# Performance work log

Hardware: AMD Instinct MI355X
Metric: run time of the kernel (lower is better)

The kernel has to match this reference:

```python
import jax, jax.numpy as jnp
import numpy as np


def setup_inputs() -> dict:
    key = jax.random.key(0)
    k1, k2 = jax.random.split(key)
    B, C_in, H, Wd = 8, 64, 64, 64
    C_a = 32
    x = jax.random.normal(k1, (B, C_in, H, Wd), dtype=jnp.float32)
    # 1x1 conv == per-pixel linear map: weight [C_a, C_in], bias [C_a]
    W = jax.random.normal(k2, (C_a, C_in), dtype=jnp.float32) * (1.0 / np.sqrt(C_in))
    b = jnp.zeros((C_a,), dtype=jnp.float32)
    return {"x": x, "W": W, "b": b}


def reference(x, W, b):
    B, C, H, Wd = x.shape
    N = H * Wd
    # g = 1x1 conv: [B, C_a, H, W] -> flatten spatial -> [B, C_a, N]
    g = jnp.einsum('oc,bchw->bohw', W, x) + b[None, :, None, None]
    g = g.reshape(B, -1, N)
    # alpha[b, n, m] = softmax_m( sum_c g[b,c,n] * g[b,c,m] )  (unscaled)
    scores = jnp.einsum('bcn,bcm->bnm', g, g)
    alpha = jax.nn.softmax(scores, axis=2)
    # r[b, c, n] = sum_m alpha[b,n,m] * x[b,c,m]
    xf = x.reshape(B, C, N)
    r = jnp.einsum('bnm,bcm->bcn', alpha, xf)
    # residual (intended semantics of is_residual=True) + ReLU epilogue
    r = r + xf
    out = jax.nn.relu(r).reshape(B, C, H, Wd)
    return (out, alpha)
```

## Files before the change

### kernel.cpp

```cpp
#include <hip/hip_runtime.h>
#include <math.h>

#define BB 8
#define CC 64
#define NA 4096
#define KA 32
#define LOG2E 1.4426950408889634f

typedef short bfrag __attribute__((ext_vector_type(8)));
typedef int   i4    __attribute__((ext_vector_type(4)));
typedef float f4    __attribute__((ext_vector_type(4)));
typedef float f16v  __attribute__((ext_vector_type(16)));

__device__ __forceinline__ f16v mf(bfrag a, bfrag b, f16v c) {
    return __builtin_amdgcn_mfma_f32_32x32x16_bf16(a, b, c, 0, 0, 0);
}

__device__ __forceinline__ unsigned short bfrne(float f) {
    unsigned u = __builtin_bit_cast(unsigned, f);
    return (unsigned short)((u + 0x7FFFu + ((u >> 16) & 1u)) >> 16);
}
__device__ __forceinline__ unsigned pk2(float a, float b) {
    return (unsigned)bfrne(a) | ((unsigned)bfrne(b) << 16);
}
__device__ __forceinline__ float bf2f(unsigned short h) {
    unsigned u = ((unsigned)h) << 16;
    return __builtin_bit_cast(float, u);
}

__global__ __launch_bounds__(256) void k_g(const float* __restrict__ x,
                                           const float* __restrict__ W,
                                           const float* __restrict__ bias,
                                           short* __restrict__ ghi,
                                           short* __restrict__ glo,
                                           float* __restrict__ norms) {
    __shared__ float Wl[KA * CC];
    __shared__ float bl[KA];
    int tid = threadIdx.x;
    for (int i = tid; i < KA * CC; i += 256) Wl[i] = W[i];
    if (tid < KA) bl[tid] = bias[tid];
    __syncthreads();

    int b = blockIdx.y;
    int n = blockIdx.x * 256 + tid;

    float acc[KA];
#pragma unroll
    for (int k = 0; k < KA; k++) acc[k] = 0.f;

    const float* xp = x + (size_t)b * CC * NA + n;
#pragma unroll 4
    for (int c = 0; c < CC; c++) {
        float xv = xp[(size_t)c * NA];
#pragma unroll
        for (int k = 0; k < KA; k++) acc[k] = fmaf(Wl[k * CC + c], xv, acc[k]);
    }

    float ss = 0.f;
    unsigned ph[KA / 2], pl[KA / 2];
#pragma unroll
    for (int k = 0; k < KA; k += 2) {
        float v0 = acc[k] + bl[k];
        float v1 = acc[k + 1] + bl[k + 1];
        ss = fmaf(v0, v0, fmaf(v1, v1, ss));
        unsigned short h0 = bfrne(v0), h1 = bfrne(v1);
        float l0 = v0 - bf2f(h0), l1 = v1 - bf2f(h1);
        ph[k / 2] = (unsigned)h0 | ((unsigned)h1 << 16);
        pl[k / 2] = (unsigned)bfrne(l0) | ((unsigned)bfrne(l1) << 16);
    }
    norms[b * NA + n] = sqrtf(ss);

    size_t row = ((size_t)b * NA + n) * KA;
#pragma unroll
    for (int q = 0; q < 4; q++) {
        i4 vh = { (int)ph[4 * q], (int)ph[4 * q + 1], (int)ph[4 * q + 2], (int)ph[4 * q + 3] };
        i4 vl = { (int)pl[4 * q], (int)pl[4 * q + 1], (int)pl[4 * q + 2], (int)pl[4 * q + 3] };
        *(i4*)(ghi + row + q * 8) = vh;
        *(i4*)(glo + row + q * 8) = vl;
    }
}

__global__ __launch_bounds__(256) void k_gmax(const float* __restrict__ norms,
                                              float* __restrict__ gmaxp) {
    int b = blockIdx.x, tid = threadIdx.x;
    float m = 0.f;
    for (int i = tid; i < NA; i += 256) m = fmaxf(m, norms[b * NA + i]);
#pragma unroll
    for (int off = 1; off < 64; off <<= 1) m = fmaxf(m, __shfl_xor(m, off));
    __shared__ float red[4];
    if ((tid & 63) == 0) red[tid >> 6] = m;
    __syncthreads();
    if (tid == 0) gmaxp[b] = fmaxf(fmaxf(red[0], red[1]), fmaxf(red[2], red[3]));
}

__global__ __launch_bounds__(256) void k_xb(const float* __restrict__ x,
                                            short* __restrict__ xb) {
    size_t idx = ((size_t)blockIdx.x * 256 + threadIdx.x) * 4;
    f4 v = *(const f4*)(x + idx);
    int2 p;
    p.x = (int)pk2(v[0], v[1]);
    p.y = (int)pk2(v[2], v[3]);
    *(int2*)(xb + idx) = p;
}

__global__ __launch_bounds__(256, 4) void k_den(const short* __restrict__ ghi,
                                                const short* __restrict__ glo,
                                                const float* __restrict__ norms,
                                                const float* __restrict__ gmaxp,
                                                float* __restrict__ partial) {
    __shared__ float rowsum[4][32];
    const int tid = threadIdx.x;
    const int w = tid >> 6;
    const int l31 = tid & 31;
    const int hi = (tid >> 5) & 1;
    const int id = blockIdx.x;
    const int b = id & 7;
    const int rr = id >> 3;
    const int nb = rr & 127;
    const int mc = rr >> 7;
    const int n0 = nb * 32;

    const float C2 = -norms[b * NA + n0 + l31] * gmaxp[b] * LOG2E;
    const short* gh = ghi + (size_t)b * NA * KA;
    const short* gl = glo + (size_t)b * NA * KA;

    bfrag Bh[2], Bl[2];
#pragma unroll
    for (int kt = 0; kt < 2; kt++) {
        size_t o = (size_t)(n0 + l31) * KA + kt * 16 + hi * 8;
        Bh[kt] = *(const bfrag*)(gh + o);
        Bl[kt] = *(const bfrag*)(gl + o);
    }

    float ls = 0.f;
#pragma unroll 2
    for (int i = 0; i < 8; i++) {
        const int m0 = (mc * 8 + i) * 128 + w * 32;
        bfrag Ah[2], Al[2];
#pragma unroll
        for (int kt = 0; kt < 2; kt++) {
            size_t o = (size_t)(m0 + l31) * KA + kt * 16 + hi * 8;
            Ah[kt] = *(const bfrag*)(gh + o);
            Al[kt] = *(const bfrag*)(gl + o);
        }
        f16v sA = {}, sB = {};
        sA = mf(Ah[0], Bh[0], sA); sA = mf(Ah[1], Bh[1], sA);
        sB = mf(Ah[0], Bl[0], sB); sB = mf(Ah[1], Bl[1], sB);
        sB = mf(Al[0], Bh[0], sB); sB = mf(Al[1], Bh[1], sB);
#pragma unroll
        for (int r = 0; r < 16; r++) ls += exp2f(fmaf(sA[r] + sB[r], LOG2E, C2));
    }
    ls += __shfl_xor(ls, 32);
    if (hi == 0) rowsum[w][l31] = ls;
    __syncthreads();
    if (tid < 32)
        partial[((size_t)mc * BB + b) * NA + n0 + tid] =
            rowsum[0][tid] + rowsum[1][tid] + rowsum[2][tid] + rowsum[3][tid];
}

__global__ __launch_bounds__(256) void k_red(const float* __restrict__ partial,
                                             float* __restrict__ linv) {
    int i = blockIdx.x * 256 + threadIdx.x;
    const size_t S = (size_t)BB * NA;
    linv[i] = 1.f / (partial[i] + partial[S + i] + partial[2 * S + i] + partial[3 * S + i]);
}

__global__ __launch_bounds__(256, 2) void k_attn2(const float* __restrict__ x,
                                                  const short* __restrict__ ghi,
                                                  const short* __restrict__ glo,
                                                  const short* __restrict__ xb,
                                                  const float* __restrict__ norms,
                                                  const float* __restrict__ gmaxp,
                                                  const float* __restrict__ linv,
                                                  float* __restrict__ out,
                                                  float* __restrict__ alpha) {
    __shared__ __align__(16) char smem[2 * 32 * 256 * 4];
    float* ast = (float*)smem;

    const int tid = threadIdx.x;
    const int w = tid >> 6;
    const int l31 = tid & 31;
    const int hi = (tid >> 5) & 1;
    const int id = blockIdx.x;
    const int b = id & 7;
    const int n0 = (id >> 3) * 32;

    const float M = norms[b * NA + n0 + l31] * gmaxp[b];
    const float C2 = -M * LOG2E;
    const float L = linv[b * NA + n0 + l31];

    const short* gh = ghi + (size_t)b * NA * KA;
    const short* gl = glo + (size_t)b * NA * KA;
    const short* xp = xb + (size_t)b * CC * NA;
    float* ap = alpha + (size_t)b * NA * NA;

    bfrag Bh[2], Bl[2];
#pragma unroll
    for (int kt = 0; kt < 2; kt++) {
        size_t o = (size_t)(n0 + l31) * KA + kt * 16 + hi * 8;
        Bh[kt] = *(const bfrag*)(gh + o);
        Bl[kt] = *(const bfrag*)(gl + o);
    }

    f16v pv0 = {}, pv1 = {};

    for (int it = 0; it < 16; ++it) {
        float* astb = ast + (it & 1) * 8192;

#pragma unroll
        for (int sub = 0; sub < 2; ++sub) {
            const int m0 = it * 256 + sub * 128 + w * 32;
            bfrag Ah[2], Al[2];
#pragma unroll
            for (int kt = 0; kt < 2; kt++) {
                size_t o = (size_t)(m0 + l31) * KA + kt * 16 + hi * 8;
                Ah[kt] = *(const bfrag*)(gh + o);
                Al[kt] = *(const bfrag*)(gl + o);
            }
            f16v sA = {}, sB = {};
            sA = mf(Ah[0], Bh[0], sA); sA = mf(Ah[1], Bh[1], sA);
            sB = mf(Ah[0], Bl[0], sB); sB = mf(Ah[1], Bl[1], sB);
            sB = mf(Al[0], Bh[0], sB); sB = mf(Al[1], Bh[1], sB);

            float a[16];
#pragma unroll
            for (int r = 0; r < 16; r++) a[r] = exp2f(fmaf(sA[r] + sB[r], LOG2E, C2)) * L;

#pragma unroll
            for (int q = 0; q < 4; q++) {
                f4 v = { a[4 * q], a[4 * q + 1], a[4 * q + 2], a[4 * q + 3] };
                int phys = (w * 8 + 2 * q + hi) ^ (l31 & 7);
                *(f4*)&astb[l31 * 256 + sub * 128 + phys * 4] = v;
            }

            unsigned p0 = pk2(a[0], a[1]),   p1 = pk2(a[2], a[3]);
            unsigned p2 = pk2(a[4], a[5]),   p3 = pk2(a[6], a[7]);
            unsigned p4 = pk2(a[8], a[9]),   p5 = pk2(a[10], a[11]);
            unsigned p6 = pk2(a[12], a[13]), p7 = pk2(a[14], a[15]);
            asm("v_permlane32_swap_b32 %0, %1" : "+v"(p0), "+v"(p2));
            asm("v_permlane32_swap_b32 %0, %1" : "+v"(p1), "+v"(p3));
            asm("v_permlane32_swap_b32 %0, %1" : "+v"(p4), "+v"(p6));
            asm("v_permlane32_swap_b32 %0, %1" : "+v"(p5), "+v"(p7));
            i4 f0 = { (int)p0, (int)p1, (int)p2, (int)p3 };
            i4 f1 = { (int)p4, (int)p5, (int)p6, (int)p7 };
            bfrag pa0 = __builtin_bit_cast(bfrag, f0);
            bfrag pa1 = __builtin_bit_cast(bfrag, f1);

            size_t ox0 = (size_t)l31 * NA + m0 + hi * 8;
            size_t ox1 = (size_t)(32 + l31) * NA + m0 + hi * 8;
            bfrag X00 = *(const bfrag*)(xp + ox0);
            bfrag X01 = *(const bfrag*)(xp + ox0 + 16);
            bfrag X10 = *(const bfrag*)(xp + ox1);
            bfrag X11 = *(const bfrag*)(xp + ox1 + 16);

            pv0 = mf(pa0, X00, pv0); pv0 = mf(pa1, X01, pv0);
            pv1 = mf(pa0, X10, pv1); pv1 = mf(pa1, X11, pv1);
        }

        __syncthreads();

#pragma unroll
        for (int e = 0; e < 8; e++) {
            int flat = e * 256 + tid;
            int row = flat >> 6;
            int c4 = flat & 63;
            int grp = c4 >> 5, c32 = c4 & 31;
            int phys = c32 ^ (row & 7);
            f4 v = *(const f4*)&astb[row * 256 + grp * 128 + phys * 4];
            __builtin_nontemporal_store(v, (f4*)(ap + (size_t)(n0 + row) * NA + it * 256 + c4 * 4));
        }
    }
    __syncthreads();

    float (*pvr0)[CC + 1] = (float(*)[CC + 1])smem;
    float (*pvr1)[CC + 1] = (float(*)[CC + 1])(smem + 32 * (CC + 1) * 4);
    if (w >= 2) {
        float (*buf)[CC + 1] = (w == 2) ? pvr0 : pvr1;
#pragma unroll
        for (int r = 0; r < 16; r++) {
            int nl = (r & 3) + 8 * (r >> 2) + 4 * hi;
            buf[nl][l31]      = pv0[r];
            buf[nl][32 + l31] = pv1[r];
        }
    }
    __syncthreads();
    if (w < 2) {
        float (*buf)[CC + 1] = (w == 0) ? pvr0 : pvr1;
#pragma unroll
        for (int r = 0; r < 16; r++) {
            int nl = (r & 3) + 8 * (r >> 2) + 4 * hi;
            buf[nl][l31]      += pv0[r];
            buf[nl][32 + l31] += pv1[r];
        }
    }
    __syncthreads();

    const float* xr = x + (size_t)b * CC * NA + n0;
    float* op = out + (size_t)b * CC * NA + n0;
#pragma unroll
    for (int e = 0; e < 8; e++) {
        int idx = e * 256 + tid;
        int c = idx >> 5, n = idx & 31;
        float v = pvr0[n][c] + pvr1[n][c] + xr[(size_t)c * NA + n];
        op[(size_t)c * NA + n] = fmaxf(v, 0.f);
    }
}

extern "C" void kernel_launch(void* const* d_in, const int* in_sizes, int n_in,
                              void* d_out, int out_size, void* d_ws, size_t ws_size,
                              hipStream_t stream) {
    const float* x = (const float*)d_in[0];
    const float* W = (const float*)d_in[1];
    const float* bias = (const float*)d_in[2];

    float* out = (float*)d_out;
    float* alpha = out + (size_t)BB * CC * NA;

    short* ghi = (short*)d_ws;
    short* glo = ghi + (size_t)BB * NA * KA;
    short* xb  = glo + (size_t)BB * NA * KA;
    float* norms = (float*)(xb + (size_t)BB * CC * NA);
    float* gmaxp = norms + (size_t)BB * NA;
    float* partial = gmaxp + BB;
    float* linv = partial + (size_t)4 * BB * NA;

    k_g<<<dim3(NA / 256, BB), 256, 0, stream>>>(x, W, bias, ghi, glo, norms);
    k_gmax<<<BB, 256, 0, stream>>>(norms, gmaxp);
    k_xb<<<(BB * CC * NA) / (256 * 4), 256, 0, stream>>>(x, xb);
    k_den<<<4096, 256, 0, stream>>>(ghi, glo, norms, gmaxp, partial);
    k_red<<<BB * NA / 256, 256, 0, stream>>>(partial, linv);
    k_attn2<<<1024, 256, 0, stream>>>(x, ghi, glo, xb, norms, gmaxp, linv, out, alpha);
}
```

Baseline: 201.4 us.

## Store alpha directly from registers, drop LDS staging, prefetch fragments, fold scale into exponent

The attention kernel no longer stages alpha tiles through a 64KB shared-memory buffer with per-iteration barriers. Each wave now writes its alpha values straight to global memory with 16-byte stores. Each wave also processes a contiguous 256-column chunk, with double-buffered register prefetch of the g and x fragments. The 1/rowsum multiply is folded into the exp2 offset via log2(L). The smaller LDS footprint allows occupancy of 3 blocks. The trade-off is that the direct stores are strided (32-byte segments per row across lanes) rather than fully coalesced row writes, and they are no longer nontemporal. Register pressure from the prefetch buffers also rises.

```diff
diff --git a/kernel.cpp b/kernel.cpp
--- a/kernel.cpp
+++ b/kernel.cpp
@@ -165,7 +165,7 @@
     linv[i] = 1.f / (partial[i] + partial[S + i] + partial[2 * S + i] + partial[3 * S + i]);
 }
 
-__global__ __launch_bounds__(256, 2) void k_attn2(const float* __restrict__ x,
+__global__ __launch_bounds__(256, 3) void k_attn2(const float* __restrict__ x,
                                                   const short* __restrict__ ghi,
                                                   const short* __restrict__ glo,
                                                   const short* __restrict__ xb,
@@ -174,8 +174,7 @@
                                                   const float* __restrict__ linv,
                                                   float* __restrict__ out,
                                                   float* __restrict__ alpha) {
-    __shared__ __align__(16) char smem[2 * 32 * 256 * 4];
-    float* ast = (float*)smem;
+    __shared__ float pvr[2][32][CC + 1];
 
     const int tid = threadIdx.x;
     const int w = tid >> 6;
@@ -186,8 +185,8 @@
     const int n0 = (id >> 3) * 32;
 
     const float M = norms[b * NA + n0 + l31] * gmaxp[b];
-    const float C2 = -M * LOG2E;
     const float L = linv[b * NA + n0 + l31];
+    const float C2L = fmaf(-M, LOG2E, __log2f(L));
 
     const short* gh = ghi + (size_t)b * NA * KA;
     const short* gl = glo + (size_t)b * NA * KA;
@@ -203,34 +202,60 @@
     }
 
     f16v pv0 = {}, pv1 = {};
-
-    for (int it = 0; it < 16; ++it) {
-        float* astb = ast + (it & 1) * 8192;
-
-#pragma unroll
-        for (int sub = 0; sub < 2; ++sub) {
-            const int m0 = it * 256 + sub * 128 + w * 32;
-            bfrag Ah[2], Al[2];
-#pragma unroll
-            for (int kt = 0; kt < 2; kt++) {
-                size_t o = (size_t)(m0 + l31) * KA + kt * 16 + hi * 8;
-                Ah[kt] = *(const bfrag*)(gh + o);
-                Al[kt] = *(const bfrag*)(gl + o);
+    float* arow = ap + (size_t)(n0 + l31) * NA + hi * 4;
+
+    for (int si = 0; si < 4; ++si) {
+        const int mbase = si * 1024 + w * 256;
+
+        bfrag A[2][4];
+        bfrag X[2][4];
+        {
+            size_t o = (size_t)(mbase + l31) * KA + hi * 8;
+            A[0][0] = *(const bfrag*)(gh + o);
+            A[0][1] = *(const bfrag*)(gh + o + 16);
+            A[0][2] = *(const bfrag*)(gl + o);
+            A[0][3] = *(const bfrag*)(gl + o + 16);
+            size_t ox0 = (size_t)l31 * NA + mbase + hi * 8;
+            size_t ox1 = (size_t)(32 + l31) * NA + mbase + hi * 8;
+            X[0][0] = *(const bfrag*)(xp + ox0);
+            X[0][1] = *(const bfrag*)(xp + ox0 + 16);
+            X[0][2] = *(const bfrag*)(xp + ox1);
+            X[0][3] = *(const bfrag*)(xp + ox1 + 16);
+        }
+
+#pragma unroll
+        for (int st = 0; st < 8; ++st) {
+            const int cur = st & 1, nxt = cur ^ 1;
+            const int m0 = mbase + st * 32;
+
+            f16v sA = {}, sB = {};
+            sA = mf(A[cur][0], Bh[0], sA); sA = mf(A[cur][1], Bh[1], sA);
+            sB = mf(A[cur][0], Bl[0], sB); sB = mf(A[cur][1], Bl[1], sB);
+            sB = mf(A[cur][2], Bh[0], sB); sB = mf(A[cur][3], Bh[1], sB);
+
+            if (st < 7) {
+                const int m1 = m0 + 32;
+                size_t o = (size_t)(m1 + l31) * KA + hi * 8;
+                A[nxt][0] = *(const bfrag*)(gh + o);
+                A[nxt][1] = *(const bfrag*)(gh + o + 16);
+                A[nxt][2] = *(const bfrag*)(gl + o);
+                A[nxt][3] = *(const bfrag*)(gl + o + 16);
+                size_t ox0 = (size_t)l31 * NA + m1 + hi * 8;
+                size_t ox1 = (size_t)(32 + l31) * NA + m1 + hi * 8;
+                X[nxt][0] = *(const bfrag*)(xp + ox0);
+                X[nxt][1] = *(const bfrag*)(xp + ox0 + 16);
+                X[nxt][2] = *(const bfrag*)(xp + ox1);
+                X[nxt][3] = *(const bfrag*)(xp + ox1 + 16);
             }
-            f16v sA = {}, sB = {};
-            sA = mf(Ah[0], Bh[0], sA); sA = mf(Ah[1], Bh[1], sA);
-            sB = mf(Ah[0], Bl[0], sB); sB = mf(Ah[1], Bl[1], sB);
-            sB = mf(Al[0], Bh[0], sB); sB = mf(Al[1], Bh[1], sB);
 
             float a[16];
 #pragma unroll
-            for (int r = 0; r < 16; r++) a[r] = exp2f(fmaf(sA[r] + sB[r], LOG2E, C2)) * L;
+            for (int r = 0; r < 16; r++) a[r] = exp2f(fmaf(sA[r] + sB[r], LOG2E, C2L));
 
 #pragma unroll
             for (int q = 0; q < 4; q++) {
                 f4 v = { a[4 * q], a[4 * q + 1], a[4 * q + 2], a[4 * q + 3] };
-                int phys = (w * 8 + 2 * q + hi) ^ (l31 & 7);
-                *(f4*)&astb[l31 * 256 + sub * 128 + phys * 4] = v;
+                *(f4*)(arow + m0 + 8 * q) = v;
             }
 
             unsigned p0 = pk2(a[0], a[1]),   p1 = pk2(a[2], a[3]);
@@ -246,36 +271,13 @@
             bfrag pa0 = __builtin_bit_cast(bfrag, f0);
             bfrag pa1 = __builtin_bit_cast(bfrag, f1);
 
-            size_t ox0 = (size_t)l31 * NA + m0 + hi * 8;
-            size_t ox1 = (size_t)(32 + l31) * NA + m0 + hi * 8;
-            bfrag X00 = *(const bfrag*)(xp + ox0);
-            bfrag X01 = *(const bfrag*)(xp + ox0 + 16);
-            bfrag X10 = *(const bfrag*)(xp + ox1);
-            bfrag X11 = *(const bfrag*)(xp + ox1 + 16);
-
-            pv0 = mf(pa0, X00, pv0); pv0 = mf(pa1, X01, pv0);
-            pv1 = mf(pa0, X10, pv1); pv1 = mf(pa1, X11, pv1);
-        }
-
-        __syncthreads();
-
-#pragma unroll
-        for (int e = 0; e < 8; e++) {
-            int flat = e * 256 + tid;
-            int row = flat >> 6;
-            int c4 = flat & 63;
-            int grp = c4 >> 5, c32 = c4 & 31;
-            int phys = c32 ^ (row & 7);
-            f4 v = *(const f4*)&astb[row * 256 + grp * 128 + phys * 4];
-            __builtin_nontemporal_store(v, (f4*)(ap + (size_t)(n0 + row) * NA + it * 256 + c4 * 4));
-        }
-    }
-    __syncthreads();
-
-    float (*pvr0)[CC + 1] = (float(*)[CC + 1])smem;
-    float (*pvr1)[CC + 1] = (float(*)[CC + 1])(smem + 32 * (CC + 1) * 4);
+            pv0 = mf(pa0, X[cur][0], pv0); pv0 = mf(pa1, X[cur][1], pv0);
+            pv1 = mf(pa0, X[cur][2], pv1); pv1 = mf(pa1, X[cur][3], pv1);
+        }
+    }
+
     if (w >= 2) {
-        float (*buf)[CC + 1] = (w == 2) ? pvr0 : pvr1;
+        float (*buf)[CC + 1] = pvr[w - 2];
 #pragma unroll
         for (int r = 0; r < 16; r++) {
             int nl = (r & 3) + 8 * (r >> 2) + 4 * hi;
@@ -285,7 +287,7 @@
     }
     __syncthreads();
     if (w < 2) {
-        float (*buf)[CC + 1] = (w == 0) ? pvr0 : pvr1;
+        float (*buf)[CC + 1] = pvr[w];
 #pragma unroll
         for (int r = 0; r < 16; r++) {
             int nl = (r & 3) + 8 * (r >> 2) + 4 * hi;
@@ -301,7 +303,7 @@
     for (int e = 0; e < 8; e++) {
         int idx = e * 256 + tid;
         int c = idx >> 5, n = idx & 31;
-        float v = pvr0[n][c] + pvr1[n][c] + xr[(size_t)c * NA + n];
+        float v = pvr[0][n][c] + pvr[1][n][c] + xr[(size_t)c * NA + n];
         op[(size_t)c * NA + n] = fmaxf(v, 0.f);
     }
 }
```

Result: slower. 282.2 us (+40.1%).

## Fuse max-norm and denominator reductions via atomics, re-layout bf16 x for attention

Applied to the files above, without the earlier changes.

Folds the per-batch max-norm reduction into the projection kernel with an atomicMax, and replaces the partial-sum buffer plus reduce kernel with atomicAdd into a row-sum zeroed in the projection kernel. This removes two kernel launches and an intermediate buffer. The softmax normalization moves into the exponent as a subtracted log2 of the row sum, which saves a multiply per element. The bf16 copy of x is transposed into a channel-interleaved layout so the attention kernel's MFMA B-fragment loads are contiguous, and the alpha store loop is remapped per wave. The max-norm slot is never reset before atomicMax, so it depends on the workspace starting at zero or holding the same value.

```diff
diff --git a/kernel.cpp b/kernel.cpp
--- a/kernel.cpp
+++ b/kernel.cpp
@@ -33,9 +33,12 @@
                                            const float* __restrict__ bias,
                                            short* __restrict__ ghi,
                                            short* __restrict__ glo,
-                                           float* __restrict__ norms) {
+                                           float* __restrict__ norms,
+                                           int* __restrict__ gmaxi,
+                                           float* __restrict__ lsum) {
     __shared__ float Wl[KA * CC];
     __shared__ float bl[KA];
+    __shared__ float red[4];
     int tid = threadIdx.x;
     for (int i = tid; i < KA * CC; i += 256) Wl[i] = W[i];
     if (tid < KA) bl[tid] = bias[tid];
@@ -68,7 +71,9 @@
         ph[k / 2] = (unsigned)h0 | ((unsigned)h1 << 16);
         pl[k / 2] = (unsigned)bfrne(l0) | ((unsigned)bfrne(l1) << 16);
     }
-    norms[b * NA + n] = sqrtf(ss);
+    float nrm = sqrtf(ss);
+    norms[b * NA + n] = nrm;
+    lsum[b * NA + n] = 0.f;
 
     size_t row = ((size_t)b * NA + n) * KA;
 #pragma unroll
@@ -78,36 +83,55 @@
         *(i4*)(ghi + row + q * 8) = vh;
         *(i4*)(glo + row + q * 8) = vl;
     }
-}
-
-__global__ __launch_bounds__(256) void k_gmax(const float* __restrict__ norms,
-                                              float* __restrict__ gmaxp) {
-    int b = blockIdx.x, tid = threadIdx.x;
-    float m = 0.f;
-    for (int i = tid; i < NA; i += 256) m = fmaxf(m, norms[b * NA + i]);
+
+    float m = nrm;
 #pragma unroll
     for (int off = 1; off < 64; off <<= 1) m = fmaxf(m, __shfl_xor(m, off));
-    __shared__ float red[4];
     if ((tid & 63) == 0) red[tid >> 6] = m;
     __syncthreads();
-    if (tid == 0) gmaxp[b] = fmaxf(fmaxf(red[0], red[1]), fmaxf(red[2], red[3]));
+    if (tid == 0) {
+        float bm = fmaxf(fmaxf(red[0], red[1]), fmaxf(red[2], red[3]));
+        atomicMax(&gmaxi[b], __float_as_int(bm));
+    }
 }
 
 __global__ __launch_bounds__(256) void k_xb(const float* __restrict__ x,
-                                            short* __restrict__ xb) {
-    size_t idx = ((size_t)blockIdx.x * 256 + threadIdx.x) * 4;
-    f4 v = *(const f4*)(x + idx);
-    int2 p;
-    p.x = (int)pk2(v[0], v[1]);
-    p.y = (int)pk2(v[2], v[3]);
-    *(int2*)(xb + idx) = p;
+                                            short* __restrict__ xb2) {
+    __shared__ float t[64][65];
+    const int tid = threadIdx.x;
+    const int b = blockIdx.y;
+    const int m0 = blockIdx.x * 64;
+
+    const int c0 = tid >> 4, m4 = (tid & 15) * 4;
+#pragma unroll
+    for (int p = 0; p < 4; p++) {
+        int c = p * 16 + c0;
+        f4 v = *(const f4*)(x + ((size_t)b * CC + c) * NA + m0 + m4);
+        t[c][m4 + 0] = v[0];
+        t[c][m4 + 1] = v[1];
+        t[c][m4 + 2] = v[2];
+        t[c][m4 + 3] = v[3];
+    }
+    __syncthreads();
+
+    short* xo = xb2 + (size_t)b * CC * NA;
+#pragma unroll
+    for (int q = 0; q < 2; q++) {
+        int idx = q * 256 + tid;
+        int mgl = idx >> 6, c = idx & 63;
+        i4 pkd;
+#pragma unroll
+        for (int j = 0; j < 4; j++)
+            pkd[j] = (int)pk2(t[c][mgl * 8 + 2 * j], t[c][mgl * 8 + 2 * j + 1]);
+        *(i4*)(xo + (size_t)(((m0 >> 3) + mgl) * 64 + c) * 8) = pkd;
+    }
 }
 
 __global__ __launch_bounds__(256, 4) void k_den(const short* __restrict__ ghi,
                                                 const short* __restrict__ glo,
                                                 const float* __restrict__ norms,
-                                                const float* __restrict__ gmaxp,
-                                                float* __restrict__ partial) {
+                                                const int* __restrict__ gmaxi,
+                                                float* __restrict__ lsum) {
     __shared__ float rowsum[4][32];
     const int tid = threadIdx.x;
     const int w = tid >> 6;
@@ -120,7 +144,8 @@
     const int mc = rr >> 7;
     const int n0 = nb * 32;
 
-    const float C2 = -norms[b * NA + n0 + l31] * gmaxp[b] * LOG2E;
+    const float gmax = __int_as_float(gmaxi[b]);
+    const float C2 = -norms[b * NA + n0 + l31] * gmax * LOG2E;
     const short* gh = ghi + (size_t)b * NA * KA;
     const short* gl = glo + (size_t)b * NA * KA;
 
@@ -154,24 +179,17 @@
     if (hi == 0) rowsum[w][l31] = ls;
     __syncthreads();
     if (tid < 32)
-        partial[((size_t)mc * BB + b) * NA + n0 + tid] =
-            rowsum[0][tid] + rowsum[1][tid] + rowsum[2][tid] + rowsum[3][tid];
-}
-
-__global__ __launch_bounds__(256) void k_red(const float* __restrict__ partial,
-                                             float* __restrict__ linv) {
-    int i = blockIdx.x * 256 + threadIdx.x;
-    const size_t S = (size_t)BB * NA;
-    linv[i] = 1.f / (partial[i] + partial[S + i] + partial[2 * S + i] + partial[3 * S + i]);
+        atomicAdd(&lsum[b * NA + n0 + tid],
+                  rowsum[0][tid] + rowsum[1][tid] + rowsum[2][tid] + rowsum[3][tid]);
 }
 
 __global__ __launch_bounds__(256, 2) void k_attn2(const float* __restrict__ x,
                                                   const short* __restrict__ ghi,
                                                   const short* __restrict__ glo,
-                                                  const short* __restrict__ xb,
+                                                  const short* __restrict__ xb2,
                                                   const float* __restrict__ norms,
-                                                  const float* __restrict__ gmaxp,
-                                                  const float* __restrict__ linv,
+                                                  const int* __restrict__ gmaxi,
+                                                  const float* __restrict__ lsum,
                                                   float* __restrict__ out,
                                                   float* __restrict__ alpha) {
     __shared__ __align__(16) char smem[2 * 32 * 256 * 4];
@@ -179,19 +197,19 @@
 
     const int tid = threadIdx.x;
     const int w = tid >> 6;
+    const int l = tid & 63;
     const int l31 = tid & 31;
     const int hi = (tid >> 5) & 1;
     const int id = blockIdx.x;
     const int b = id & 7;
     const int n0 = (id >> 3) * 32;
 
-    const float M = norms[b * NA + n0 + l31] * gmaxp[b];
-    const float C2 = -M * LOG2E;
-    const float L = linv[b * NA + n0 + l31];
+    const float M = norms[b * NA + n0 + l31] * __int_as_float(gmaxi[b]);
+    const float C2L = fmaf(-M, LOG2E, -__log2f(lsum[b * NA + n0 + l31]));
 
     const short* gh = ghi + (size_t)b * NA * KA;
     const short* gl = glo + (size_t)b * NA * KA;
-    const short* xp = xb + (size_t)b * CC * NA;
+    const short* xp = xb2 + (size_t)b * CC * NA;
     float* ap = alpha + (size_t)b * NA * NA;
 
     bfrag Bh[2], Bl[2];
@@ -224,7 +242,7 @@
 
             float a[16];
 #pragma unroll
-            for (int r = 0; r < 16; r++) a[r] = exp2f(fmaf(sA[r] + sB[r], LOG2E, C2)) * L;
+            for (int r = 0; r < 16; r++) a[r] = exp2f(fmaf(sA[r] + sB[r], LOG2E, C2L));
 
 #pragma unroll
             for (int q = 0; q < 4; q++) {
@@ -246,12 +264,11 @@
             bfrag pa0 = __builtin_bit_cast(bfrag, f0);
             bfrag pa1 = __builtin_bit_cast(bfrag, f1);
 
-            size_t ox0 = (size_t)l31 * NA + m0 + hi * 8;
-            size_t ox1 = (size_t)(32 + l31) * NA + m0 + hi * 8;
-            bfrag X00 = *(const bfrag*)(xp + ox0);
-            bfrag X01 = *(const bfrag*)(xp + ox0 + 16);
-            bfrag X10 = *(const bfrag*)(xp + ox1);
-            bfrag X11 = *(const bfrag*)(xp + ox1 + 16);
+            const int mg = m0 >> 3;
+            bfrag X00 = *(const bfrag*)(xp + (size_t)((mg + hi) * 64 + l31) * 8);
+            bfrag X01 = *(const bfrag*)(xp + (size_t)((mg + 2 + hi) * 64 + l31) * 8);
+            bfrag X10 = *(const bfrag*)(xp + (size_t)((mg + hi) * 64 + 32 + l31) * 8);
+            bfrag X11 = *(const bfrag*)(xp + (size_t)((mg + 2 + hi) * 64 + 32 + l31) * 8);
 
             pv0 = mf(pa0, X00, pv0); pv0 = mf(pa1, X01, pv0);
             pv1 = mf(pa0, X10, pv1); pv1 = mf(pa1, X11, pv1);
@@ -261,12 +278,10 @@
 
 #pragma unroll
         for (int e = 0; e < 8; e++) {
-            int flat = e * 256 + tid;
-            int row = flat >> 6;
-            int c4 = flat & 63;
-            int grp = c4 >> 5, c32 = c4 & 31;
-            int phys = c32 ^ (row & 7);
-            f4 v = *(const f4*)&astb[row * 256 + grp * 128 + phys * 4];
+            int row = w * 8 + e;
+            int c4 = l;
+            int phys = (c4 & 31) ^ e;
+            f4 v = *(const f4*)&astb[row * 256 + (c4 >> 5) * 128 + phys * 4];
             __builtin_nontemporal_store(v, (f4*)(ap + (size_t)(n0 + row) * NA + it * 256 + c4 * 4));
         }
     }
@@ -318,16 +333,13 @@
 
     short* ghi = (short*)d_ws;
     short* glo = ghi + (size_t)BB * NA * KA;
-    short* xb  = glo + (size_t)BB * NA * KA;
-    float* norms = (float*)(xb + (size_t)BB * CC * NA);
-    float* gmaxp = norms + (size_t)BB * NA;
-    float* partial = gmaxp + BB;
-    float* linv = partial + (size_t)4 * BB * NA;
-
-    k_g<<<dim3(NA / 256, BB), 256, 0, stream>>>(x, W, bias, ghi, glo, norms);
-    k_gmax<<<BB, 256, 0, stream>>>(norms, gmaxp);
-    k_xb<<<(BB * CC * NA) / (256 * 4), 256, 0, stream>>>(x, xb);
-    k_den<<<4096, 256, 0, stream>>>(ghi, glo, norms, gmaxp, partial);
-    k_red<<<BB * NA / 256, 256, 0, stream>>>(partial, linv);
-    k_attn2<<<1024, 256, 0, stream>>>(x, ghi, glo, xb, norms, gmaxp, linv, out, alpha);
-}
+    short* xb2 = glo + (size_t)BB * NA * KA;
+    float* norms = (float*)(xb2 + (size_t)BB * CC * NA);
+    int*   gmaxi = (int*)(norms + (size_t)BB * NA);
+    float* lsum  = (float*)(gmaxi + 8);
+
+    k_g<<<dim3(NA / 256, BB), 256, 0, stream>>>(x, W, bias, ghi, glo, norms, gmaxi, lsum);
+    k_xb<<<dim3(NA / 64, BB), 256, 0, stream>>>(x, xb2);
+    k_den<<<4096, 256, 0, stream>>>(ghi, glo, norms, gmaxi, lsum);
+    k_attn2<<<1024, 256, 0, stream>>>(x, ghi, glo, xb2, norms, gmaxi, lsum, out, alpha);
+}
```

New measurement: 181.3 us. 1.11x faster.
